# Kernel optimization log

Hardware: AMD Instinct MI355X
Metric: run time of the kernel (lower is better)

The kernel has to match this reference:

```python
import jax, jax.numpy as jnp
import numpy as np

H_DIM = 128
C_DIM = 128


def _linear_params(key, in_dim, out_dim):
    kw, kb = jax.random.split(key)
    bound = 1.0 / np.sqrt(in_dim)
    W = jax.random.uniform(kw, (in_dim, out_dim), minval=-bound, maxval=bound, dtype=jnp.float32)
    b = jax.random.uniform(kb, (out_dim,), minval=-bound, maxval=bound, dtype=jnp.float32)
    return W, b


def setup_inputs() -> dict:
    key = jax.random.key(0)
    kx, kh, kc, k1, k2, k3, k4, k5 = jax.random.split(key, 8)
    B = 262144
    x = jax.random.normal(kx, (B, H_DIM), dtype=jnp.float32)
    h = jax.random.normal(kh, (B, H_DIM), dtype=jnp.float32)
    c = jax.random.normal(kc, (B, C_DIM), dtype=jnp.float32)
    Wf, bf = _linear_params(k1, 2 * H_DIM, H_DIM)
    Wi, bi = _linear_params(k2, 2 * H_DIM, H_DIM)
    Wc, bc = _linear_params(k3, 2 * H_DIM, C_DIM)
    Wo, bo = _linear_params(k4, 2 * H_DIM, H_DIM)
    Wch, bch = _linear_params(k5, C_DIM, H_DIM)
    return {"x": x, "h": h, "c": c,
            "Wf": Wf, "bf": bf, "Wi": Wi, "bi": bi,
            "Wc": Wc, "bc": bc, "Wo": Wo, "bo": bo,
            "Wch": Wch, "bch": bch}


def reference(x, h, c, Wf, bf, Wi, bi, Wc, bc, Wo, bo, Wch, bch):
    concat = jnp.concatenate([x, h], axis=-1)  # [B, 2H]
    # Fuse the four gate projections into one GEMM, then split.
    W_gates = jnp.concatenate([Wf, Wi, Wc, Wo], axis=1)  # [2H, 3H+C]
    b_gates = jnp.concatenate([bf, bi, bc, bo], axis=0)
    gates = concat @ W_gates + b_gates
    f_pre, i_pre, ct_pre, o_pre = jnp.split(
        gates, [H_DIM, 2 * H_DIM, 2 * H_DIM + C_DIM], axis=-1)
    f = jax.nn.sigmoid(f_pre)
    i = jax.nn.sigmoid(i_pre)
    c_tilde = jnp.tanh(ct_pre)
    c_new = f * c + i * c_tilde
    o = jax.nn.sigmoid(o_pre)
    h_new = o * jnp.tanh(c_new @ Wch + bch)
    return (h_new, c_new)
```

## Files before the change

kernel.cpp:

```cpp
#include <hip/hip_runtime.h>
#include <hip/hip_bf16.h>


typedef __attribute__((ext_vector_type(8))) short bf16x8;
typedef __attribute__((ext_vector_type(4))) float f32x4;

static __device__ __forceinline__ unsigned short f2bf(float f) {
    unsigned int u = __builtin_bit_cast(unsigned int, f);
    u += 0x7FFFu + ((u >> 16) & 1u);
    return (unsigned short)(u >> 16);
}

static __device__ __forceinline__ bf16x8 cvt8(f32x4 a, f32x4 b) {
    union { bf16x8 v; unsigned short u[8]; } r;
    r.u[0] = f2bf(a[0]); r.u[1] = f2bf(a[1]); r.u[2] = f2bf(a[2]); r.u[3] = f2bf(a[3]);
    r.u[4] = f2bf(b[0]); r.u[5] = f2bf(b[1]); r.u[6] = f2bf(b[2]); r.u[7] = f2bf(b[3]);
    return r.v;
}

static __device__ __forceinline__ float fsig(float x) {
    float e = __builtin_amdgcn_exp2f(-1.44269504f * x);
    return __builtin_amdgcn_rcpf(1.0f + e);
}
static __device__ __forceinline__ float ftanh(float x) {
    float e = __builtin_amdgcn_exp2f(2.8853900818f * x);
    return 1.0f - 2.0f * __builtin_amdgcn_rcpf(e + 1.0f);
}

__global__ void prep_weights(const float* __restrict__ Wf, const float* __restrict__ Wi,
                             const float* __restrict__ Wc, const float* __restrict__ Wo,
                             const float* __restrict__ Wch,
                             unsigned short* __restrict__ WgF,
                             unsigned short* __restrict__ WchF)
{
    int u = blockIdx.x * 256 + threadIdx.x;
    if (u < 16384) {
        int lane = u & 63, g = (u >> 6) & 3, wn = (u >> 8) & 7, ks = u >> 11;
        int l15 = lane & 15, lg = lane >> 4;
        int cg = wn * 16 + l15;
        int k0 = ks * 32 + lg * 8;
        const float* W = (g == 0) ? Wf : (g == 1) ? Wi : (g == 2) ? Wc : Wo;
        union { bf16x8 v; unsigned short s[8]; } r;
#pragma unroll
        for (int i = 0; i < 8; ++i) r.s[i] = f2bf(W[(size_t)(k0 + i) * 128 + cg]);
        *(bf16x8*)(WgF + (size_t)u * 8) = r.v;
    } else if (u < 16384 + 2048) {
        int u2 = u - 16384;
        int lane = u2 & 63, wn = (u2 >> 6) & 7, kt = u2 >> 9;
        int l15 = lane & 15, lg = lane >> 4;
        int col = wn * 16 + l15, k0 = kt * 32 + lg * 8;
        union { bf16x8 v; unsigned short s[8]; } r;
#pragma unroll
        for (int i = 0; i < 8; ++i) r.s[i] = f2bf(Wch[(size_t)(k0 + i) * 128 + col]);
        *(bf16x8*)(WchF + (size_t)u2 * 8) = r.v;
    }
}

__global__ __launch_bounds__(512, 2) void lstm_fused(
    const float* __restrict__ xg, const float* __restrict__ hg, const float* __restrict__ cg,
    const float* __restrict__ bfv, const float* __restrict__ biv,
    const float* __restrict__ bcv, const float* __restrict__ bov,
    const float* __restrict__ bchv,
    const unsigned short* __restrict__ WgF, const unsigned short* __restrict__ WchF,
    float* __restrict__ out, int nrows)
{
    __shared__ uint4 lds4[3072];
    char* lds = (char*)lds4;

    const int tid  = threadIdx.x;
    const int lane = tid & 63;
    const int wn   = tid >> 6;
    const int l15  = lane & 15;
    const int lg   = lane >> 4;
    const long base = (long)blockIdx.x << 10;

    float* hout = out;
    float* cout = out + (size_t)nrows * 128;

    const int colc = wn * 16 + l15;
    const float bfb = bfv[colc], bib = biv[colc], bcb = bcv[colc],
                bob = bov[colc], bchb = bchv[colc];

    bf16x8 Breg[8][4];
#pragma unroll
    for (int ks = 0; ks < 8; ++ks)
#pragma unroll
        for (int g = 0; g < 4; ++g)
            Breg[ks][g] = *(const bf16x8*)(WgF + (size_t)((ks * 32 + wn * 4 + g) * 512 + lane * 8));
    bf16x8 Wreg[4];
#pragma unroll
    for (int kt = 0; kt < 4; ++kt)
        Wreg[kt] = *(const bf16x8*)(WchF + (size_t)((kt * 8 + wn) * 512 + lane * 8));

    const int rowA = tid >> 4;
    const int kgA  = tid & 15;
    const int ksA  = kgA >> 1;
    const int lgA  = (kgA & 1) * 2;
    const int amA  = rowA >> 4;
    const int l15A = rowA & 15;
    const int aoff0 = (amA * 8 + ksA) * 1024 + ((((lgA    ) * 16 + l15A) * 16) ^ (ksA << 4));
    const int aoff1 = (amA * 8 + ksA) * 1024 + ((((lgA + 1) * 16 + l15A) * 16) ^ (ksA << 4));
    const float* asrc = (kgA < 8) ? (xg + kgA * 16) : (hg + (kgA - 8) * 16);

    {
        const float* s = asrc + (base + rowA) * 128;
        f32x4 v0 = ((const f32x4*)s)[0], v1 = ((const f32x4*)s)[1],
              v2 = ((const f32x4*)s)[2], v3 = ((const f32x4*)s)[3];
        *(bf16x8*)(lds + aoff0) = cvt8(v0, v1);
        *(bf16x8*)(lds + aoff1) = cvt8(v2, v3);
    }
    float creg[8];
#pragma unroll
    for (int am = 0; am < 2; ++am)
#pragma unroll
        for (int r = 0; r < 4; ++r)
            creg[am * 4 + r] = cg[(base + am * 16 + lg * 4 + r) * 128 + colc];
    __syncthreads();

    f32x4 acc[2][4];
#pragma unroll
    for (int am = 0; am < 2; ++am)
#pragma unroll
        for (int g = 0; g < 4; ++g) acc[am][g] = {0.f, 0.f, 0.f, 0.f};

    for (int t = 0; t < 32; ++t) {
        const int cur = t & 1;
        const long m0 = base + t * 32;

        f32x4 a0, a1, a2, a3;
        if (t < 31) {
            const float* s = asrc + (m0 + 32 + rowA) * 128;
            a0 = ((const f32x4*)s)[0]; a1 = ((const f32x4*)s)[1];
            a2 = ((const f32x4*)s)[2]; a3 = ((const f32x4*)s)[3];
        }
        float cregN[8];
        if (t < 31) {
#pragma unroll
            for (int am = 0; am < 2; ++am)
#pragma unroll
                for (int r = 0; r < 4; ++r)
                    cregN[am * 4 + r] = cg[(m0 + 32 + am * 16 + lg * 4 + r) * 128 + colc];
        }
        const char* ab = lds + cur * 16384;
#pragma unroll
        for (int ks = 0; ks < 8; ++ks) {
            bf16x8 af0 = *(const bf16x8*)(ab + (ks       ) * 1024 + ((lane * 16) ^ (ks << 4)));
            bf16x8 af1 = *(const bf16x8*)(ab + (8 + ks   ) * 1024 + ((lane * 16) ^ (ks << 4)));
#pragma unroll
            for (int g = 0; g < 4; ++g) {
                acc[0][g] = __builtin_amdgcn_mfma_f32_16x16x32_bf16(af0, Breg[ks][g], acc[0][g], 0, 0, 0);
                acc[1][g] = __builtin_amdgcn_mfma_f32_16x16x32_bf16(af1, Breg[ks][g], acc[1][g], 0, 0, 0);
            }
        }
        char* cex = lds + 32768 + cur * 8192;
        const int cslotbase = ((wn & 1) * 2 + (l15 >> 3)) * 16;
#pragma unroll
        for (int am = 0; am < 2; ++am)
#pragma unroll
            for (int r = 0; r < 4; ++r) {
                float f  = fsig(acc[am][0][r] + bfb);
                float i  = fsig(acc[am][1][r] + bib);
                float ct = ftanh(acc[am][2][r] + bcb);
                float cv = f * creg[am * 4 + r] + i * ct;
                cout[(m0 + am * 16 + lg * 4 + r) * 128 + colc] = cv;
                *(unsigned short*)(cex + (am * 4 + (wn >> 1)) * 1024
                                       + (cslotbase + lg * 4 + r) * 16 + (l15 & 7) * 2) = f2bf(cv);
            }
        if (t < 31) {
            char* fb = lds + (cur ^ 1) * 16384;
            *(bf16x8*)(fb + aoff0) = cvt8(a0, a1);
            *(bf16x8*)(fb + aoff1) = cvt8(a2, a3);
        }
        asm volatile("s_waitcnt lgkmcnt(0)" ::: "memory");
        __builtin_amdgcn_s_barrier();
        __builtin_amdgcn_sched_barrier(0);
        f32x4 acc2_0 = {0.f, 0.f, 0.f, 0.f}, acc2_1 = {0.f, 0.f, 0.f, 0.f};
#pragma unroll
        for (int kt = 0; kt < 4; ++kt) {
            bf16x8 p0 = *(const bf16x8*)(cex + (kt    ) * 1024 + lane * 16);
            bf16x8 p1 = *(const bf16x8*)(cex + (4 + kt) * 1024 + lane * 16);
            acc2_0 = __builtin_amdgcn_mfma_f32_16x16x32_bf16(p0, Wreg[kt], acc2_0, 0, 0, 0);
            acc2_1 = __builtin_amdgcn_mfma_f32_16x16x32_bf16(p1, Wreg[kt], acc2_1, 0, 0, 0);
        }
#pragma unroll
        for (int r = 0; r < 4; ++r) {
            float o0 = fsig(acc[0][3][r] + bob);
            hout[(m0 +      lg * 4 + r) * 128 + colc] = o0 * ftanh(acc2_0[r] + bchb);
            float o1 = fsig(acc[1][3][r] + bob);
            hout[(m0 + 16 + lg * 4 + r) * 128 + colc] = o1 * ftanh(acc2_1[r] + bchb);
        }
#pragma unroll
        for (int am = 0; am < 2; ++am)
#pragma unroll
            for (int g = 0; g < 4; ++g) acc[am][g] = {0.f, 0.f, 0.f, 0.f};
        if (t < 31) {
#pragma unroll
            for (int q = 0; q < 8; ++q) creg[q] = cregN[q];
        }
    }
}

extern "C" void kernel_launch(void* const* d_in, const int* in_sizes, int n_in,
                              void* d_out, int out_size, void* d_ws, size_t ws_size,
                              hipStream_t stream)
{
    const float* x   = (const float*)d_in[0];
    const float* h   = (const float*)d_in[1];
    const float* c   = (const float*)d_in[2];
    const float* Wf  = (const float*)d_in[3];
    const float* bf_ = (const float*)d_in[4];
    const float* Wi  = (const float*)d_in[5];
    const float* bi_ = (const float*)d_in[6];
    const float* Wc  = (const float*)d_in[7];
    const float* bc_ = (const float*)d_in[8];
    const float* Wo  = (const float*)d_in[9];
    const float* bo_ = (const float*)d_in[10];
    const float* Wch = (const float*)d_in[11];
    const float* bch = (const float*)d_in[12];

    unsigned short* WgF  = (unsigned short*)d_ws;
    unsigned short* WchF = WgF + 512 * 256;
    float* out = (float*)d_out;

    int nrows = in_sizes[0] / 128;

    prep_weights<<<dim3(72), dim3(256), 0, stream>>>(Wf, Wi, Wc, Wo, Wch, WgF, WchF);
    lstm_fused<<<dim3(nrows / 1024), dim3(512), 0, stream>>>(
        x, h, c, bf_, bi_, bc_, bo_, bch, WgF, WchF, out, nrows);
}
```

Measured before the change: 147.6 us.

## Prefetch A tiles two steps ahead with ping-pong registers and packed bf16 convert

The main loop is unrolled by two with rotating register sets, so global loads of x/h rows are issued two tiles ahead instead of one. This gives memory latency a longer window to hide behind the MFMA work. The fp32-to-bf16 conversion of A tiles now uses the hardware packed v_cvt_pk_bf16_f32 instruction instead of manual rounding. The cost is a second set of prefetch registers, which may raise register pressure under launch_bounds(512,2).

```diff
diff --git a/kernel.cpp b/kernel.cpp
--- a/kernel.cpp
+++ b/kernel.cpp
@@ -11,10 +11,18 @@
     return (unsigned short)(u >> 16);
 }
 
+static __device__ __forceinline__ unsigned int cvtpk(float lo, float hi) {
+    unsigned int r;
+    asm("v_cvt_pk_bf16_f32 %0, %1, %2" : "=v"(r) : "v"(lo), "v"(hi));
+    return r;
+}
+
 static __device__ __forceinline__ bf16x8 cvt8(f32x4 a, f32x4 b) {
-    union { bf16x8 v; unsigned short u[8]; } r;
-    r.u[0] = f2bf(a[0]); r.u[1] = f2bf(a[1]); r.u[2] = f2bf(a[2]); r.u[3] = f2bf(a[3]);
-    r.u[4] = f2bf(b[0]); r.u[5] = f2bf(b[1]); r.u[6] = f2bf(b[2]); r.u[7] = f2bf(b[3]);
+    union { bf16x8 v; unsigned int w[4]; } r;
+    r.w[0] = cvtpk(a[0], a[1]);
+    r.w[1] = cvtpk(a[2], a[3]);
+    r.w[2] = cvtpk(b[0], b[1]);
+    r.w[3] = cvtpk(b[2], b[3]);
     return r.v;
 }
 
@@ -56,6 +64,85 @@
     }
 }
 
+#define TILE_BODY(T, CUR, RI0,RI1,RI2,RI3, RO0,RO1,RO2,RO3, CIN, COUT)          \
+  do {                                                                          \
+    const long m0 = base + (long)(T) * 32;                                      \
+                                   \
+    if ((T) < 30) {                                                             \
+      const float* s_ = asrc + (m0 + 64 + rowA) * 128;                          \
+      RO0 = ((const f32x4*)s_)[0]; RO1 = ((const f32x4*)s_)[1];                 \
+      RO2 = ((const f32x4*)s_)[2]; RO3 = ((const f32x4*)s_)[3];                 \
+    }                                                                           \
+                                             \
+    if ((T) < 31) {                                                             \
+      _Pragma("unroll")                                                         \
+      for (int am = 0; am < 2; ++am)                                            \
+        _Pragma("unroll")                                                       \
+        for (int r = 0; r < 4; ++r)                                             \
+          COUT[am * 4 + r] = cg[(m0 + 32 + am * 16 + lg * 4 + r) * 128 + colc]; \
+    }                                                                           \
+                 \
+    {                                                                           \
+      const char* ab = lds + (CUR) * 16384;                                     \
+      _Pragma("unroll")                                                         \
+      for (int ks = 0; ks < 8; ++ks) {                                          \
+        bf16x8 af0 = *(const bf16x8*)(ab + ks * 1024 + ((lane * 16) ^ (ks << 4)));       \
+        bf16x8 af1 = *(const bf16x8*)(ab + (8 + ks) * 1024 + ((lane * 16) ^ (ks << 4))); \
+        _Pragma("unroll")                                                       \
+        for (int g_ = 0; g_ < 4; ++g_) {                                        \
+          acc[0][g_] = __builtin_amdgcn_mfma_f32_16x16x32_bf16(af0, Breg[ks][g_], acc[0][g_], 0, 0, 0); \
+          acc[1][g_] = __builtin_amdgcn_mfma_f32_16x16x32_bf16(af1, Breg[ks][g_], acc[1][g_], 0, 0, 0); \
+        }                                                                       \
+      }                                                                         \
+    }                                                                           \
+       \
+    char* cex = lds + 32768 + (CUR) * 8192;                                     \
+    _Pragma("unroll")                                                           \
+    for (int am = 0; am < 2; ++am)                                              \
+      _Pragma("unroll")                                                         \
+      for (int r = 0; r < 4; ++r) {                                             \
+        float f_  = fsig(acc[am][0][r] + bfb);                                  \
+        float i_  = fsig(acc[am][1][r] + bib);                                  \
+        float ct_ = ftanh(acc[am][2][r] + bcb);                                 \
+        float cv_ = f_ * CIN[am * 4 + r] + i_ * ct_;                            \
+        coutp[(m0 + am * 16 + lg * 4 + r) * 128 + colc] = cv_;                  \
+        *(unsigned short*)(cex + (am * 4 + (wn >> 1)) * 1024                    \
+             + (cslotbase + lg * 4 + r) * 16 + (l15 & 7) * 2) = f2bf(cv_);      \
+      }                                                                         \
+                                  \
+    if ((T) < 31) {                                                             \
+      char* fb = lds + ((CUR) ^ 1) * 16384;                                     \
+      *(bf16x8*)(fb + aoff0) = cvt8(RI0, RI1);                                  \
+      *(bf16x8*)(fb + aoff1) = cvt8(RI2, RI3);                                  \
+    }                                                                           \
+         \
+    asm volatile("s_waitcnt lgkmcnt(0)" ::: "memory");                          \
+    __builtin_amdgcn_s_barrier();                                               \
+    __builtin_amdgcn_sched_barrier(0);                                          \
+                               \
+    {                                                                           \
+      f32x4 acc2_0 = {0.f,0.f,0.f,0.f}, acc2_1 = {0.f,0.f,0.f,0.f};             \
+      _Pragma("unroll")                                                         \
+      for (int kt = 0; kt < 4; ++kt) {                                          \
+        bf16x8 p0 = *(const bf16x8*)(cex + kt * 1024 + lane * 16);              \
+        bf16x8 p1 = *(const bf16x8*)(cex + (4 + kt) * 1024 + lane * 16);        \
+        acc2_0 = __builtin_amdgcn_mfma_f32_16x16x32_bf16(p0, Wreg[kt], acc2_0, 0, 0, 0); \
+        acc2_1 = __builtin_amdgcn_mfma_f32_16x16x32_bf16(p1, Wreg[kt], acc2_1, 0, 0, 0); \
+      }                                                                         \
+      _Pragma("unroll")                                                         \
+      for (int r = 0; r < 4; ++r) {                                             \
+        float o0 = fsig(acc[0][3][r] + bob);                                    \
+        houtp[(m0 +      lg * 4 + r) * 128 + colc] = o0 * ftanh(acc2_0[r] + bchb); \
+        float o1 = fsig(acc[1][3][r] + bob);                                    \
+        houtp[(m0 + 16 + lg * 4 + r) * 128 + colc] = o1 * ftanh(acc2_1[r] + bchb); \
+      }                                                                         \
+    }                                                                           \
+    _Pragma("unroll")                                                           \
+    for (int am = 0; am < 2; ++am)                                              \
+      _Pragma("unroll")                                                         \
+      for (int g_ = 0; g_ < 4; ++g_) acc[am][g_] = (f32x4){0.f,0.f,0.f,0.f};    \
+  } while (0)
+
 __global__ __launch_bounds__(512, 2) void lstm_fused(
     const float* __restrict__ xg, const float* __restrict__ hg, const float* __restrict__ cg,
     const float* __restrict__ bfv, const float* __restrict__ biv,
@@ -74,12 +161,13 @@
     const int lg   = lane >> 4;
     const long base = (long)blockIdx.x << 10;
 
-    float* hout = out;
-    float* cout = out + (size_t)nrows * 128;
+    float* houtp = out;
+    float* coutp = out + (size_t)nrows * 128;
 
     const int colc = wn * 16 + l15;
     const float bfb = bfv[colc], bib = biv[colc], bcb = bcv[colc],
                 bob = bov[colc], bchb = bchv[colc];
+    const int cslotbase = ((wn & 1) * 2 + (l15 >> 3)) * 16;
 
     bf16x8 Breg[8][4];
 #pragma unroll
@@ -109,12 +197,18 @@
         *(bf16x8*)(lds + aoff0) = cvt8(v0, v1);
         *(bf16x8*)(lds + aoff1) = cvt8(v2, v3);
     }
-    float creg[8];
+    f32x4 rA0, rA1, rA2, rA3, rB0, rB1, rB2, rB3;
+    {
+        const float* s = asrc + (base + 32 + rowA) * 128;
+        rA0 = ((const f32x4*)s)[0]; rA1 = ((const f32x4*)s)[1];
+        rA2 = ((const f32x4*)s)[2]; rA3 = ((const f32x4*)s)[3];
+    }
+    float c0[8], c1[8];
 #pragma unroll
     for (int am = 0; am < 2; ++am)
 #pragma unroll
         for (int r = 0; r < 4; ++r)
-            creg[am * 4 + r] = cg[(base + am * 16 + lg * 4 + r) * 128 + colc];
+            c0[am * 4 + r] = cg[(base + am * 16 + lg * 4 + r) * 128 + colc];
     __syncthreads();
 
     f32x4 acc[2][4];
@@ -123,80 +217,10 @@
 #pragma unroll
         for (int g = 0; g < 4; ++g) acc[am][g] = {0.f, 0.f, 0.f, 0.f};
 
-    for (int t = 0; t < 32; ++t) {
-        const int cur = t & 1;
-        const long m0 = base + t * 32;
-
-        f32x4 a0, a1, a2, a3;
-        if (t < 31) {
-            const float* s = asrc + (m0 + 32 + rowA) * 128;
-            a0 = ((const f32x4*)s)[0]; a1 = ((const f32x4*)s)[1];
-            a2 = ((const f32x4*)s)[2]; a3 = ((const f32x4*)s)[3];
-        }
-        float cregN[8];
-        if (t < 31) {
-#pragma unroll
-            for (int am = 0; am < 2; ++am)
-#pragma unroll
-                for (int r = 0; r < 4; ++r)
-                    cregN[am * 4 + r] = cg[(m0 + 32 + am * 16 + lg * 4 + r) * 128 + colc];
-        }
-        const char* ab = lds + cur * 16384;
-#pragma unroll
-        for (int ks = 0; ks < 8; ++ks) {
-            bf16x8 af0 = *(const bf16x8*)(ab + (ks       ) * 1024 + ((lane * 16) ^ (ks << 4)));
-            bf16x8 af1 = *(const bf16x8*)(ab + (8 + ks   ) * 1024 + ((lane * 16) ^ (ks << 4)));
-#pragma unroll
-            for (int g = 0; g < 4; ++g) {
-                acc[0][g] = __builtin_amdgcn_mfma_f32_16x16x32_bf16(af0, Breg[ks][g], acc[0][g], 0, 0, 0);
-                acc[1][g] = __builtin_amdgcn_mfma_f32_16x16x32_bf16(af1, Breg[ks][g], acc[1][g], 0, 0, 0);
-            }
-        }
-        char* cex = lds + 32768 + cur * 8192;
-        const int cslotbase = ((wn & 1) * 2 + (l15 >> 3)) * 16;
-#pragma unroll
-        for (int am = 0; am < 2; ++am)
-#pragma unroll
-            for (int r = 0; r < 4; ++r) {
-                float f  = fsig(acc[am][0][r] + bfb);
-                float i  = fsig(acc[am][1][r] + bib);
-                float ct = ftanh(acc[am][2][r] + bcb);
-                float cv = f * creg[am * 4 + r] + i * ct;
-                cout[(m0 + am * 16 + lg * 4 + r) * 128 + colc] = cv;
-                *(unsigned short*)(cex + (am * 4 + (wn >> 1)) * 1024
-                                       + (cslotbase + lg * 4 + r) * 16 + (l15 & 7) * 2) = f2bf(cv);
-            }
-        if (t < 31) {
-            char* fb = lds + (cur ^ 1) * 16384;
-            *(bf16x8*)(fb + aoff0) = cvt8(a0, a1);
-            *(bf16x8*)(fb + aoff1) = cvt8(a2, a3);
-        }
-        asm volatile("s_waitcnt lgkmcnt(0)" ::: "memory");
-        __builtin_amdgcn_s_barrier();
-        __builtin_amdgcn_sched_barrier(0);
-        f32x4 acc2_0 = {0.f, 0.f, 0.f, 0.f}, acc2_1 = {0.f, 0.f, 0.f, 0.f};
-#pragma unroll
-        for (int kt = 0; kt < 4; ++kt) {
-            bf16x8 p0 = *(const bf16x8*)(cex + (kt    ) * 1024 + lane * 16);
-            bf16x8 p1 = *(const bf16x8*)(cex + (4 + kt) * 1024 + lane * 16);
-            acc2_0 = __builtin_amdgcn_mfma_f32_16x16x32_bf16(p0, Wreg[kt], acc2_0, 0, 0, 0);
-            acc2_1 = __builtin_amdgcn_mfma_f32_16x16x32_bf16(p1, Wreg[kt], acc2_1, 0, 0, 0);
-        }
-#pragma unroll
-        for (int r = 0; r < 4; ++r) {
-            float o0 = fsig(acc[0][3][r] + bob);
-            hout[(m0 +      lg * 4 + r) * 128 + colc] = o0 * ftanh(acc2_0[r] + bchb);
-            float o1 = fsig(acc[1][3][r] + bob);
-            hout[(m0 + 16 + lg * 4 + r) * 128 + colc] = o1 * ftanh(acc2_1[r] + bchb);
-        }
-#pragma unroll
-        for (int am = 0; am < 2; ++am)
-#pragma unroll
-            for (int g = 0; g < 4; ++g) acc[am][g] = {0.f, 0.f, 0.f, 0.f};
-        if (t < 31) {
-#pragma unroll
-            for (int q = 0; q < 8; ++q) creg[q] = cregN[q];
-        }
+#pragma unroll 1
+    for (int t = 0; t < 32; t += 2) {
+        TILE_BODY(t,     0, rA0,rA1,rA2,rA3, rB0,rB1,rB2,rB3, c0, c1);
+        TILE_BODY(t + 1, 1, rB0,rB1,rB2,rB3, rA0,rA1,rA2,rA3, c1, c0);
     }
 }
 
```

New measurement: 278.8 us. 88.9% more time.
